# Optimization experiments

Hardware: AMD Instinct MI355X
Metric: run time of the kernel (lower is better)

## Reference

```python
import jax, jax.numpy as jnp
import numpy as np

D_MODEL = 1024
D_INNER = 1024
N_HEADS = 16
HEAD_DIM = D_INNER // N_HEADS  # 64
D_STATE = 16
DT_RANK = 16
CHUNK = 64
PROJ = 2 * D_INNER + 2 * D_STATE * N_HEADS + DT_RANK  # 2576


def setup_inputs() -> dict:
    key = jax.random.key(0)
    ks = jax.random.split(key, 6)
    B, S = 4, 4096
    x = jax.random.normal(ks[0], (B, S, D_MODEL), jnp.float32)
    W_in = jax.random.normal(ks[1], (PROJ, D_MODEL), jnp.float32) * 0.02
    dt_W = jax.random.normal(ks[2], (N_HEADS, DT_RANK), jnp.float32) * 0.1
    dt_b = jax.random.normal(ks[3], (N_HEADS,), jnp.float32) * 0.1
    A_log = jnp.full((N_HEADS,), jnp.log(0.5), jnp.float32)
    D_param = jnp.ones((N_HEADS,), jnp.float32)
    W_out = jax.random.normal(ks[4], (D_MODEL, D_INNER), jnp.float32) * 0.02
    norm_w = jnp.ones((D_INNER,), jnp.float32)
    return dict(x=x, W_in=W_in, dt_W=dt_W, dt_b=dt_b, A_log=A_log,
                D_param=D_param, W_out=W_out, norm_w=norm_w)


def _forward(x, W_in, dt_W, dt_b, A_log, D_param, W_out, norm_w):
    B, S, _ = x.shape
    H, P, N, K = N_HEADS, HEAD_DIM, D_STATE, CHUNK
    proj = x @ W_in.T  # (B,S,PROJ)
    xp = proj[..., :D_INNER]
    z = proj[..., D_INNER:2 * D_INNER]
    o = 2 * D_INNER
    B_ssm = proj[..., o:o + N * H].reshape(B, S, H, N)
    C_ssm = proj[..., o + N * H:o + 2 * N * H].reshape(B, S, H, N)
    dt_low = proj[..., o + 2 * N * H:]
    dt = jax.nn.softplus(dt_low @ dt_W.T + dt_b)  # (B,S,H)
    xp = xp.reshape(B, S, H, P)
    A = -jnp.exp(A_log)  # (H,)

    # --- chunked selective scan (SSD) ---
    nC = S // K  # S chosen divisible by K (original pads otherwise)
    xc = xp.reshape(B, nC, K, H, P)
    dtc = dt.reshape(B, nC, K, H)
    Bc = B_ssm.reshape(B, nC, K, H, N)
    Cc = C_ssm.reshape(B, nC, K, H, N)
    dA = dtc * A  # (B,nC,K,H)
    dAcs = jnp.cumsum(dA, axis=2)
    # intra-chunk quadratic (attention-like) form
    Lm = jnp.exp(dAcs[:, :, :, None, :] - dAcs[:, :, None, :, :])
    causal = jnp.tril(jnp.ones((K, K), jnp.float32))
    Lm = Lm * causal[None, None, :, :, None]
    scores = jnp.einsum('bcihn,bcjhn->bcijh', Cc, Bc) * Lm * dtc[:, :, None, :, :]
    y_intra = jnp.einsum('bcijh,bcjhp->bcihp', scores, xc)
    # per-chunk state contribution
    decay_to_end = jnp.exp(dAcs[:, :, -1:, :] - dAcs)
    wx = (dtc * decay_to_end)[..., None] * xc  # (B,nC,K,H,P)
    chunk_state = jnp.einsum('bckhn,bckhp->bchnp', Bc, wx)  # (B,nC,H,N,P)
    chunk_decay = jnp.exp(dAcs[:, :, -1, :])  # (B,nC,H)

    # cross-chunk recurrence: emit state at chunk START (matches torch loop)
    def step(h, inp):
        d, s = inp
        return d[:, :, None, None] * h + s, h
    h0 = jnp.zeros((B, H, N, P), jnp.float32)
    _, h_states = jax.lax.scan(
        step, h0,
        (jnp.moveaxis(chunk_decay, 1, 0), jnp.moveaxis(chunk_state, 1, 0)))
    h_states = jnp.moveaxis(h_states, 0, 1)  # (B,nC,H,N,P)

    y_cross = jnp.einsum('bcthn,bchnp,bcth->bcthp', Cc, h_states, jnp.exp(dAcs))
    y = (y_intra + y_cross).reshape(B, S, H, P)
    # --- end scan ---

    y = y + xp * D_param[None, None, :, None]
    y = y.reshape(B, S, D_INNER)
    rms = jnp.sqrt(jnp.mean(y * y, axis=-1, keepdims=True) + 1e-6)
    y = y / rms * norm_w
    y = y * jax.nn.silu(z)
    return y @ W_out.T


def reference(x, W_in, dt_W, dt_b, A_log, D_param, W_out, norm_w):
    return _forward(x, W_in, dt_W, dt_b, A_log, D_param, W_out, norm_w)
```

## Files before the change

kernel.cpp:

```cpp
#include <hip/hip_runtime.h>

typedef unsigned short u16;
typedef __attribute__((ext_vector_type(8))) short short8;
typedef __attribute__((ext_vector_type(4))) float f32x4;
typedef __attribute__((ext_vector_type(4))) unsigned short u16x4;
typedef __attribute__((ext_vector_type(8))) unsigned short u16x8;

#define BTOK 16384
#define PROJ_N 2576
#define PROJ_PAD 2816
#define DK 1024
#define NCH 256
#define NH 16
#define HD 64
#define NS 16

__device__ __forceinline__ float b2f(u16 b) {
    union { unsigned int u; float f; } v; v.u = ((unsigned int)b) << 16; return v.f;
}
__device__ __forceinline__ u16 f2b(float f) {
    union { float f; unsigned int u; } v; v.f = f;
    unsigned int r = v.u + 0x7fffu + ((v.u >> 16) & 1u);
    return (u16)(r >> 16);
}

__device__ __forceinline__ void stage_asm(const u16* g, const u16* l) {
    unsigned loff = (unsigned)(size_t)(const __attribute__((address_space(3))) u16*)l;
    unsigned su = __builtin_amdgcn_readfirstlane(loff);
    asm volatile("s_mov_b32 m0, %1\n\t"
                 "global_load_lds_dwordx4 %0, off"
                 :: "v"(g), "s"(su));
}

template <int IMM>
__device__ __forceinline__ short8 dsr128(unsigned a) {
    short8 d;
    asm volatile("ds_read_b128 %0, %1 offset:%2" : "=v"(d) : "v"(a), "i"(IMM));
    return d;
}

#define LGKM(n) do { asm volatile("s_waitcnt lgkmcnt(" #n ")"); __builtin_amdgcn_sched_barrier(0); } while (0)
#define MFMA_B16 __builtin_amdgcn_mfma_f32_16x16x32_bf16

__global__ __launch_bounds__(256) void cast_bf16(const float* __restrict__ s,
                                                 u16* __restrict__ d, int n4) {
    int t = blockIdx.x * 256 + threadIdx.x;
    if (t < n4) {
        float4 v = ((const float4*)s)[t];
        u16x4 o; o.x = f2b(v.x); o.y = f2b(v.y); o.z = f2b(v.z); o.w = f2b(v.w);
        ((u16x4*)d)[t] = o;
    }
}

__global__ __launch_bounds__(256) void cast_pad_win(const float* __restrict__ s,
                                                    u16* __restrict__ d) {
    int t = blockIdx.x * 256 + threadIdx.x;
    int i4 = t * 4;
    float4 v = make_float4(0.f, 0.f, 0.f, 0.f);
    if (i4 < PROJ_N * DK) v = ((const float4*)s)[t];
    u16x4 o; o.x = f2b(v.x); o.y = f2b(v.y); o.z = f2b(v.z); o.w = f2b(v.w);
    ((u16x4*)d)[t] = o;
}

#define MT 64

template <int OUT_BF16>
__global__ __launch_bounds__(512, 2) void gemmk(const u16* __restrict__ A,
                                                const u16* __restrict__ B,
                                                float* __restrict__ Cf,
                                                u16* __restrict__ Cb,
                                                int K, int ldc) {
    extern __shared__ u16 smem[];
    u16* AsU = smem;
    const int tid = threadIdx.x;
    const int wave = tid >> 6, lane = tid & 63;
    const int wr = wave >> 2, wc = wave & 3;
    const int m_l = lane & 15, quad = lane >> 4;

    const int b = blockIdx.x;
    const int bm = (b & 7) * 8 + ((b >> 3) & 7);
    const int bn = b >> 6;

    const u16* Ab = A + (long)bm * 256 * K;
    const u16* Bb = B + (long)bn * 256 * K;

    const unsigned lds0 = (unsigned)(size_t)(const __attribute__((address_space(3))) u16*)smem;
    const int sw = m_l & 7;
    const unsigned a0b = lds0 + (wr * 128 + m_l) * 128 + (quad ^ sw) * 16;
    const unsigned a1b = lds0 + (wr * 128 + m_l) * 128 + ((4 + quad) ^ sw) * 16;
    const unsigned b0b = lds0 + 65536 + (wc * 64 + m_l) * 128 + (quad ^ sw) * 16;
    const unsigned b1b = lds0 + 65536 + (wc * 64 + m_l) * 128 + ((4 + quad) ^ sw) * 16;

    const int srow = tid >> 3;
    const int schk = (tid & 7) ^ (srow & 7);
    const int sdst = wave * 512;

    f32x4 acc[8][4];
#pragma unroll
    for (int f = 0; f < 8; ++f)
#pragma unroll
        for (int n = 0; n < 4; ++n) acc[f][n] = (f32x4){0.f, 0.f, 0.f, 0.f};

    const int NT = K >> 6;

    auto stage = [&](const u16* G, u16* L, int q, int k0) {
        stage_asm(G + (long)(q * 64 + srow) * K + k0 + schk * 8,
                  L + q * 4096 + sdst);
    };
    u16* BsU = smem + 32768;

    stage(Ab, AsU, 0, 0); stage(Ab, AsU, 1, 0); stage(Ab, AsU, 2, 0); stage(Ab, AsU, 3, 0);
    stage(Bb, BsU, 0, 0); stage(Bb, BsU, 1, 0); stage(Bb, BsU, 2, 0); stage(Bb, BsU, 3, 0);
    asm volatile("s_waitcnt vmcnt(0)");
    __builtin_amdgcn_s_barrier();

    short8 afX[4], afY[4], bfX[4], bfY[4];
    afX[0] = dsr128<0>(a0b);    afX[1] = dsr128<2048>(a0b);
    afX[2] = dsr128<4096>(a0b); afX[3] = dsr128<6144>(a0b);
    bfX[0] = dsr128<0>(b0b);    bfX[1] = dsr128<2048>(b0b);
    bfX[2] = dsr128<4096>(b0b); bfX[3] = dsr128<6144>(b0b);

    int cur = 0;
    for (int t = 0; t < NT; ++t) {
        const unsigned cB = ((unsigned)cur) << 15;
        const unsigned a0 = a0b + cB, a1 = a1b + cB, b0 = b0b + cB, b1 = b1b + cB;
        const int nbu = (cur << 14) ^ 16384;
        u16* Anxt = AsU + nbu;
        u16* Bnxt = BsU + nbu;
        const int k1 = (t + 1) << 6;
        const bool s1 = (t + 1 < NT);

        if (s1) { stage(Ab, Anxt, 0, k1); stage(Ab, Anxt, 1, k1); }
        afY[0] = dsr128<8192>(a0);  afY[1] = dsr128<10240>(a0);
        afY[2] = dsr128<12288>(a0); afY[3] = dsr128<14336>(a0);
        LGKM(4);
        __builtin_amdgcn_s_setprio(1);
#pragma unroll
        for (int f = 0; f < 4; ++f)
#pragma unroll
            for (int n = 0; n < 4; ++n)
                acc[f][n] = MFMA_B16(afX[f], bfX[n], acc[f][n], 0, 0, 0);
        __builtin_amdgcn_s_setprio(0);

        if (s1) { stage(Ab, Anxt, 2, k1); stage(Ab, Anxt, 3, k1); }
        afX[0] = dsr128<0>(a1);    afX[1] = dsr128<2048>(a1);
        afX[2] = dsr128<4096>(a1); afX[3] = dsr128<6144>(a1);
        bfY[0] = dsr128<0>(b1);    bfY[1] = dsr128<2048>(b1);
        bfY[2] = dsr128<4096>(b1); bfY[3] = dsr128<6144>(b1);
        LGKM(8);
        __builtin_amdgcn_s_setprio(1);
#pragma unroll
        for (int f = 0; f < 4; ++f)
#pragma unroll
            for (int n = 0; n < 4; ++n)
                acc[4 + f][n] = MFMA_B16(afY[f], bfX[n], acc[4 + f][n], 0, 0, 0);
        __builtin_amdgcn_s_setprio(0);

        if (s1) { stage(Bb, Bnxt, 0, k1); stage(Bb, Bnxt, 1, k1); }
        afY[0] = dsr128<8192>(a1);  afY[1] = dsr128<10240>(a1);
        afY[2] = dsr128<12288>(a1); afY[3] = dsr128<14336>(a1);
        LGKM(4);
        __builtin_amdgcn_s_setprio(1);
#pragma unroll
        for (int f = 0; f < 4; ++f)
#pragma unroll
            for (int n = 0; n < 4; ++n)
                acc[f][n] = MFMA_B16(afX[f], bfY[n], acc[f][n], 0, 0, 0);
        __builtin_amdgcn_s_setprio(0);

        if (s1) { stage(Bb, Bnxt, 2, k1); stage(Bb, Bnxt, 3, k1); }
        LGKM(0);
        __builtin_amdgcn_s_setprio(1);
#pragma unroll
        for (int f = 0; f < 4; ++f)
#pragma unroll
            for (int n = 0; n < 4; ++n)
                acc[4 + f][n] = MFMA_B16(afY[f], bfY[n], acc[4 + f][n], 0, 0, 0);
        __builtin_amdgcn_s_setprio(0);
        __builtin_amdgcn_sched_barrier(0);

        if (s1) {
            asm volatile("s_waitcnt vmcnt(0)");
            __builtin_amdgcn_s_barrier();
            const unsigned nB = cB ^ 32768u;
            const unsigned na0 = a0b + nB, nb0 = b0b + nB;
            afX[0] = dsr128<0>(na0);    afX[1] = dsr128<2048>(na0);
            afX[2] = dsr128<4096>(na0); afX[3] = dsr128<6144>(na0);
            bfX[0] = dsr128<0>(nb0);    bfX[1] = dsr128<2048>(nb0);
            bfX[2] = dsr128<4096>(nb0); bfX[3] = dsr128<6144>(nb0);
        }
        cur ^= 1;
    }

#pragma unroll
    for (int f = 0; f < 8; ++f) {
        int row_base = bm * 256 + wr * 128 + f * 16 + quad * 4;
#pragma unroll
        for (int n = 0; n < 4; ++n) {
            int col = bn * 256 + wc * 64 + n * 16 + m_l;
#pragma unroll
            for (int r = 0; r < 4; ++r) {
                float v = acc[f][n][r];
                long off = (long)(row_base + r) * ldc + col;
                if (OUT_BF16) Cb[off] = f2b(v);
                else          Cf[off] = v;
            }
        }
    }
}

__global__ __launch_bounds__(256) void ssm_intra(const u16* __restrict__ proj,
                                                 const float* __restrict__ dt_W,
                                                 const float* __restrict__ dt_b,
                                                 const float* __restrict__ A_log,
                                                 float* __restrict__ dAcs,
                                                 float* __restrict__ decay,
                                                 u16* __restrict__ y_acc,
                                                 float* __restrict__ cstate) {
    int bch = blockIdx.x;
    int bc = bch >> 4, h = bch & 15;
    long tok0 = (long)bc * 64;
    __shared__ float Cs[64][20], Bm[64][20];
    __shared__ u16 Sh[64][72], Sl[64][72];
    __shared__ u16 Xt[64][72];
    __shared__ u16 Wh[64][72], Wl[64][72];
    __shared__ u16 Bt[16][72];
    __shared__ float dts[64], dAs[64], wk[64];
    const int tid = threadIdx.x;
    const int wave = tid >> 6, lane = tid & 63;
    const int m_l = lane & 15, quad = lane >> 4;

    if (tid < 64) {
        long tok = tok0 + tid;
        u16x8 lo0 = *(const u16x8*)&proj[tok * PROJ_PAD + 2560];
        u16x8 lo1 = *(const u16x8*)&proj[tok * PROJ_PAD + 2568];
        float a = dt_b[h];
#pragma unroll
        for (int r = 0; r < 8; ++r) a += b2f(lo0[r]) * dt_W[h * 16 + r];
#pragma unroll
        for (int r = 0; r < 8; ++r) a += b2f(lo1[r]) * dt_W[h * 16 + 8 + r];
        float d = (a > 20.f) ? a : log1pf(__expf(a));
        float dA = -__expf(A_log[h]) * d;
        float cs = dA;
#pragma unroll
        for (int off = 1; off < 64; off <<= 1) {
            float o = __shfl_up(cs, off, 64);
            if (tid >= off) cs += o;
        }
        float cs63 = __shfl(cs, 63, 64);
        dts[tid] = d;
        dAs[tid] = cs;
        wk[tid] = d * __expf(cs63 - cs);
        dAcs[tok * 16 + h] = cs;
        if (tid == 63) decay[bc * 16 + h] = __expf(cs);
    }
#pragma unroll
    for (int it = 0; it < 4; ++it) {
        int li = it * 256 + tid;
        int i = li >> 4, n = li & 15;
        u16 cb = proj[(tok0 + i) * PROJ_PAD + 2304 + h * 16 + n];
        u16 bb = proj[(tok0 + i) * PROJ_PAD + 2048 + h * 16 + n];
        Cs[i][n] = b2f(cb);
        Bm[i][n] = b2f(bb);
        Bt[n][i] = bb;
    }
    __syncthreads();
#pragma unroll
    for (int it = 0; it < 2; ++it) {
        int li = it * 256 + tid;
        int j = li & 63, p0 = (li >> 6) * 8;
        u16x8 xv = *(const u16x8*)&proj[(tok0 + j) * PROJ_PAD + h * 64 + p0];
        float w = wk[j];
#pragma unroll
        for (int t = 0; t < 8; ++t) {
            u16 xb = xv[t];
            Xt[p0 + t][j] = xb;
            float v = w * b2f(xb);
            u16 hi = f2b(v);
            Wh[p0 + t][j] = hi;
            Wl[p0 + t][j] = f2b(v - b2f(hi));
        }
    }
    {
        int j = tid & 63, i0 = tid >> 6;
#pragma unroll
        for (int g = 0; g < 16; ++g) {
            int i = i0 + g * 4;
            float v = 0.f;
            if (j <= i) {
                float d = 0.f;
                const f32x4* cp = (const f32x4*)Cs[i];
                const f32x4* bp = (const f32x4*)Bm[j];
#pragma unroll
                for (int n4 = 0; n4 < 4; ++n4) {
                    f32x4 c = cp[n4], b = bp[n4];
                    d += c.x * b.x + c.y * b.y + c.z * b.z + c.w * b.w;
                }
                v = d * __expf(dAs[i] - dAs[j]) * dts[j];
            }
            u16 hi = f2b(v);
            Sh[i][j] = hi;
            Sl[i][j] = f2b(v - b2f(hi));
        }
    }
    __syncthreads();
    {
        f32x4 yv[4];
#pragma unroll
        for (int jt = 0; jt < 4; ++jt) yv[jt] = (f32x4){0.f, 0.f, 0.f, 0.f};
#pragma unroll
        for (int ks = 0; ks < 2; ++ks) {
            int kc = ks * 32 + quad * 8;
            short8 ah = *(const short8*)&Sh[wave * 16 + m_l][kc];
            short8 al = *(const short8*)&Sl[wave * 16 + m_l][kc];
#pragma unroll
            for (int jt = 0; jt < 4; ++jt) {
                short8 bx = *(const short8*)&Xt[jt * 16 + m_l][kc];
                yv[jt] = MFMA_B16(ah, bx, yv[jt], 0, 0, 0);
                yv[jt] = MFMA_B16(al, bx, yv[jt], 0, 0, 0);
            }
        }
#pragma unroll
        for (int jt = 0; jt < 4; ++jt)
#pragma unroll
            for (int r = 0; r < 4; ++r) {
                int i = wave * 16 + quad * 4 + r;
                int p = jt * 16 + m_l;
                y_acc[(tok0 + i) * 1024 + h * 64 + p] = f2b(yv[jt][r]);
            }
    }
    {
        f32x4 cacc = (f32x4){0.f, 0.f, 0.f, 0.f};
#pragma unroll
        for (int ks = 0; ks < 2; ++ks) {
            int kc = ks * 32 + quad * 8;
            short8 a = *(const short8*)&Bt[m_l][kc];
            short8 bh = *(const short8*)&Wh[wave * 16 + m_l][kc];
            short8 bl = *(const short8*)&Wl[wave * 16 + m_l][kc];
            cacc = MFMA_B16(a, bh, cacc, 0, 0, 0);
            cacc = MFMA_B16(a, bl, cacc, 0, 0, 0);
        }
#pragma unroll
        for (int r = 0; r < 4; ++r) {
            int n = quad * 4 + r;
            int p = wave * 16 + m_l;
            cstate[(long)bch * 1024 + n * 64 + p] = cacc[r];
        }
    }
}

__global__ __launch_bounds__(256) void scan_chunks(const float* __restrict__ cs,
                                                   const float* __restrict__ decay,
                                                   float* __restrict__ hs) {
    int t = blockIdx.x * 256 + threadIdx.x;
    int p = t & 63, n = (t >> 6) & 15, h = (t >> 10) & 15, b = t >> 14;
    float state = 0.f;
    for (int c = 0; c < 64; ++c) {
        long idx = (((long)((b * 64 + c) * 16 + h)) * 16 + n) * 64 + p;
        hs[idx] = state;
        state = decay[(b * 64 + c) * 16 + h] * state + cs[idx];
    }
}

__global__ __launch_bounds__(256) void ssm_cross(const u16* __restrict__ proj,
                                                 const float* __restrict__ dAcs,
                                                 const float* __restrict__ hs,
                                                 const u16* __restrict__ y_acc,
                                                 const float* __restrict__ D_param,
                                                 u16* __restrict__ y_pre) {
    int bch = blockIdx.x;
    int bc = bch >> 4, h = bch & 15;
    long tok0 = (long)bc * 64;
    __shared__ float hss[16][64], Cs[64][16], dAs[64];
    int tid = threadIdx.x;
#pragma unroll
    for (int it = 0; it < 4; ++it) {
        int li = it * 256 + tid;
        hss[li >> 6][li & 63] = hs[(long)bch * 1024 + li];
        int i = li >> 4, n = li & 15;
        Cs[i][n] = b2f(proj[(tok0 + i) * PROJ_PAD + 2304 + h * 16 + n]);
    }
    if (tid < 64) dAs[tid] = dAcs[(tok0 + tid) * 16 + h];
    __syncthreads();
    float Dh = D_param[h];
    int pi = (tid & 15) * 4;
    int ib = tid >> 4;
#pragma unroll
    for (int g = 0; g < 4; ++g) {
        int i = ib + 16 * g;
        f32x4 cr = (f32x4){0.f, 0.f, 0.f, 0.f};
#pragma unroll
        for (int n = 0; n < 16; ++n) {
            float c = Cs[i][n];
            cr += c * *(const f32x4*)&hss[n][pi];
        }
        float e = __expf(dAs[i]);
        long off = (tok0 + i) * 1024 + h * 64 + pi;
        u16x4 ya = *(const u16x4*)&y_acc[off];
        u16x4 xv = *(const u16x4*)&proj[(tok0 + i) * PROJ_PAD + h * 64 + pi];
        u16x4 o;
        o.x = f2b(b2f(ya.x) + e * cr.x + b2f(xv.x) * Dh);
        o.y = f2b(b2f(ya.y) + e * cr.y + b2f(xv.y) * Dh);
        o.z = f2b(b2f(ya.z) + e * cr.z + b2f(xv.z) * Dh);
        o.w = f2b(b2f(ya.w) + e * cr.w + b2f(xv.w) * Dh);
        *(u16x4*)&y_pre[off] = o;
    }
}

__global__ __launch_bounds__(256) void norm_gate(const u16* __restrict__ proj,
                                                 const float* __restrict__ norm_w,
                                                 u16* __restrict__ y) {
    long tok = blockIdx.x;
    int tid = threadIdx.x;
    int c0 = tid * 4;
    u16x4 yv = *(const u16x4*)&y[tok * 1024 + c0];
    float v0 = b2f(yv.x), v1 = b2f(yv.y), v2 = b2f(yv.z), v3 = b2f(yv.w);
    float ss = v0 * v0 + v1 * v1 + v2 * v2 + v3 * v3;
    int lane = tid & 63, w = tid >> 6;
#pragma unroll
    for (int d = 32; d > 0; d >>= 1) ss += __shfl_down(ss, d, 64);
    __shared__ float red[4];
    if (lane == 0) red[w] = ss;
    __syncthreads();
    float tot = red[0] + red[1] + red[2] + red[3];
    float inv = rsqrtf(tot * (1.f / 1024.f) + 1e-6f);
    float4 nw = *(const float4*)&norm_w[c0];
    u16x4 zv = *(const u16x4*)&proj[tok * PROJ_PAD + 1024 + c0];
    float z0 = b2f(zv.x), z1 = b2f(zv.y), z2 = b2f(zv.z), z3 = b2f(zv.w);
    u16x4 o;
    o.x = f2b(v0 * inv * nw.x * (z0 / (1.f + __expf(-z0))));
    o.y = f2b(v1 * inv * nw.y * (z1 / (1.f + __expf(-z1))));
    o.z = f2b(v2 * inv * nw.z * (z2 / (1.f + __expf(-z2))));
    o.w = f2b(v3 * inv * nw.w * (z3 / (1.f + __expf(-z3))));
    *(u16x4*)&y[tok * 1024 + c0] = o;
}

extern "C" void kernel_launch(void* const* d_in, const int* in_sizes, int n_in,
                              void* d_out, int out_size, void* d_ws, size_t ws_size,
                              hipStream_t stream) {
    const float* x      = (const float*)d_in[0];
    const float* W_in   = (const float*)d_in[1];
    const float* dt_W   = (const float*)d_in[2];
    const float* dt_b   = (const float*)d_in[3];
    const float* A_log  = (const float*)d_in[4];
    const float* D_par  = (const float*)d_in[5];
    const float* W_out  = (const float*)d_in[6];
    const float* norm_w = (const float*)d_in[7];
    float* out = (float*)d_out;

    char* ws = (char*)d_ws;
    size_t off = 0;
    auto alloc = [&](size_t b) { void* p = ws + off; off += (b + 255) & ~(size_t)255; return p; };
    u16*   x_bf    = (u16*)alloc((size_t)BTOK * DK * 2);
    u16*   win_bf  = (u16*)alloc((size_t)PROJ_PAD * DK * 2);
    u16*   wout_bf = (u16*)alloc((size_t)DK * DK * 2);
    u16*   proj    = (u16*)alloc((size_t)BTOK * PROJ_PAD * 2);
    float* dAcs    = (float*)alloc((size_t)BTOK * NH * 4);
    float* decay   = (float*)alloc((size_t)NCH * NH * 4);
    float* cstate  = (float*)alloc((size_t)NCH * NH * NS * HD * 4);
    float* hstates = (float*)alloc((size_t)NCH * NH * NS * HD * 4);
    u16*   y_pre   = (u16*)alloc((size_t)BTOK * DK * 2);
    u16*   y_acc   = x_bf;

    static bool attr_done = false;
    if (!attr_done) {
        (void)hipFuncSetAttribute(reinterpret_cast<const void*>(&gemmk<1>),
                                  hipFuncAttributeMaxDynamicSharedMemorySize, 131072);
        (void)hipFuncSetAttribute(reinterpret_cast<const void*>(&gemmk<0>),
                                  hipFuncAttributeMaxDynamicSharedMemorySize, 131072);
        attr_done = true;
    }

    cast_bf16<<<BTOK * DK / 4 / 256, 256, 0, stream>>>(x, x_bf, BTOK * DK / 4);
    cast_bf16<<<DK * DK / 4 / 256, 256, 0, stream>>>(W_out, wout_bf, DK * DK / 4);
    cast_pad_win<<<PROJ_PAD * DK / 4 / 256, 256, 0, stream>>>(W_in, win_bf);

    gemmk<1><<<dim3(MT * (PROJ_PAD / 256)), 512, 131072, stream>>>(x_bf, win_bf, nullptr, proj, DK, PROJ_PAD);

    ssm_intra<<<NCH * NH, 256, 0, stream>>>(proj, dt_W, dt_b, A_log, dAcs, decay, y_acc, cstate);
    scan_chunks<<<256, 256, 0, stream>>>(cstate, decay, hstates);
    ssm_cross<<<NCH * NH, 256, 0, stream>>>(proj, dAcs, hstates, y_acc, D_par, y_pre);
    norm_gate<<<BTOK, 256, 0, stream>>>(proj, norm_w, y_pre);

    gemmk<0><<<dim3(MT * (DK / 256)), 512, 131072, stream>>>(y_pre, wout_bf, out, nullptr, DK, DK);
}
```

Baseline: 379.0 us.

## Load GEMM A fragments directly from global and shrink tile to 256x128

Replaces the 512-thread 256x256 GEMM, which staged both A and B tiles through 128KB of dynamic LDS, with a 256-thread 256x128 kernel. Each wave now reads its A fragments straight from global memory into registers, and only B goes through a 32KB static LDS double buffer. The projection padding drops from 2816 to 2688 columns so the grid divides by 128, which removes wasted padded compute. The intent is to cut LDS traffic, lower LDS use so more blocks can be resident, and reduce padding work. The cost is uncoalesced, un-shared A loads from global, where each A row segment is fetched by separate waves and blocks, plus less reuse per block.

```diff
diff --git a/kernel.cpp b/kernel.cpp
--- a/kernel.cpp
+++ b/kernel.cpp
@@ -8,7 +8,7 @@
 
 #define BTOK 16384
 #define PROJ_N 2576
-#define PROJ_PAD 2816
+#define PROJ_PAD 2688
 #define DK 1024
 #define NCH 256
 #define NH 16
@@ -41,6 +41,7 @@
 
 #define LGKM(n) do { asm volatile("s_waitcnt lgkmcnt(" #n ")"); __builtin_amdgcn_sched_barrier(0); } while (0)
 #define MFMA_B16 __builtin_amdgcn_mfma_f32_16x16x32_bf16
+#define SB0() __builtin_amdgcn_sched_barrier(0)
 
 __global__ __launch_bounds__(256) void cast_bf16(const float* __restrict__ s,
                                                  u16* __restrict__ d, int n4) {
@@ -65,16 +66,15 @@
 #define MT 64
 
 template <int OUT_BF16>
-__global__ __launch_bounds__(512, 2) void gemmk(const u16* __restrict__ A,
+__global__ __launch_bounds__(256, 2) void gemmf(const u16* __restrict__ A,
                                                 const u16* __restrict__ B,
                                                 float* __restrict__ Cf,
                                                 u16* __restrict__ Cb,
                                                 int K, int ldc) {
-    extern __shared__ u16 smem[];
-    u16* AsU = smem;
+    __shared__ u16 Bs[2 * 128 * 64];
     const int tid = threadIdx.x;
     const int wave = tid >> 6, lane = tid & 63;
-    const int wr = wave >> 2, wc = wave & 3;
+    const int mw = wave >> 1, nw = wave & 1;
     const int m_l = lane & 15, quad = lane >> 4;
 
     const int b = blockIdx.x;
@@ -82,18 +82,18 @@
     const int bn = b >> 6;
 
     const u16* Ab = A + (long)bm * 256 * K;
-    const u16* Bb = B + (long)bn * 256 * K;
-
-    const unsigned lds0 = (unsigned)(size_t)(const __attribute__((address_space(3))) u16*)smem;
+    const u16* Bb = B + (long)bn * 128 * K;
+
+    const u16* ap0 = Ab + (long)(mw * 128 + m_l) * K + quad * 8;
+    const int fstride = 16 * K;
+
+    const unsigned lds0 = (unsigned)(size_t)(const __attribute__((address_space(3))) u16*)Bs;
     const int sw = m_l & 7;
-    const unsigned a0b = lds0 + (wr * 128 + m_l) * 128 + (quad ^ sw) * 16;
-    const unsigned a1b = lds0 + (wr * 128 + m_l) * 128 + ((4 + quad) ^ sw) * 16;
-    const unsigned b0b = lds0 + 65536 + (wc * 64 + m_l) * 128 + (quad ^ sw) * 16;
-    const unsigned b1b = lds0 + 65536 + (wc * 64 + m_l) * 128 + ((4 + quad) ^ sw) * 16;
+    const unsigned b0b = lds0 + (nw * 64 + m_l) * 128 + (quad ^ sw) * 16;
+    const unsigned b1b = lds0 + (nw * 64 + m_l) * 128 + ((4 + quad) ^ sw) * 16;
 
     const int srow = tid >> 3;
     const int schk = (tid & 7) ^ (srow & 7);
-    const int sdst = wave * 512;
 
     f32x4 acc[8][4];
 #pragma unroll
@@ -103,101 +103,73 @@
 
     const int NT = K >> 6;
 
-    auto stage = [&](const u16* G, u16* L, int q, int k0) {
-        stage_asm(G + (long)(q * 64 + srow) * K + k0 + schk * 8,
-                  L + q * 4096 + sdst);
+    auto stageB = [&](unsigned bufU16, int q, int k0) {
+        stage_asm(Bb + (long)(q * 32 + srow) * K + k0 + schk * 8,
+                  Bs + bufU16 + q * 2048 + wave * 512);
     };
-    u16* BsU = smem + 32768;
-
-    stage(Ab, AsU, 0, 0); stage(Ab, AsU, 1, 0); stage(Ab, AsU, 2, 0); stage(Ab, AsU, 3, 0);
-    stage(Bb, BsU, 0, 0); stage(Bb, BsU, 1, 0); stage(Bb, BsU, 2, 0); stage(Bb, BsU, 3, 0);
+
+    stageB(0, 0, 0); stageB(0, 1, 0); stageB(0, 2, 0); stageB(0, 3, 0);
     asm volatile("s_waitcnt vmcnt(0)");
     __builtin_amdgcn_s_barrier();
 
-    short8 afX[4], afY[4], bfX[4], bfY[4];
-    afX[0] = dsr128<0>(a0b);    afX[1] = dsr128<2048>(a0b);
-    afX[2] = dsr128<4096>(a0b); afX[3] = dsr128<6144>(a0b);
+    short8 afX[8], afY[8], bfX[4], bfY[4];
     bfX[0] = dsr128<0>(b0b);    bfX[1] = dsr128<2048>(b0b);
     bfX[2] = dsr128<4096>(b0b); bfX[3] = dsr128<6144>(b0b);
-
-    int cur = 0;
+#pragma unroll
+    for (int f = 0; f < 8; ++f) afX[f] = *(const short8*)(ap0 + f * fstride);
+
+    unsigned curB = 0;
     for (int t = 0; t < NT; ++t) {
-        const unsigned cB = ((unsigned)cur) << 15;
-        const unsigned a0 = a0b + cB, a1 = a1b + cB, b0 = b0b + cB, b1 = b1b + cB;
-        const int nbu = (cur << 14) ^ 16384;
-        u16* Anxt = AsU + nbu;
-        u16* Bnxt = BsU + nbu;
-        const int k1 = (t + 1) << 6;
         const bool s1 = (t + 1 < NT);
-
-        if (s1) { stage(Ab, Anxt, 0, k1); stage(Ab, Anxt, 1, k1); }
-        afY[0] = dsr128<8192>(a0);  afY[1] = dsr128<10240>(a0);
-        afY[2] = dsr128<12288>(a0); afY[3] = dsr128<14336>(a0);
+        const int k0 = t << 6, k1 = (t + 1) << 6;
+
+        bfY[0] = dsr128<0>(b1b + curB);    bfY[1] = dsr128<2048>(b1b + curB);
+        bfY[2] = dsr128<4096>(b1b + curB); bfY[3] = dsr128<6144>(b1b + curB);
+#pragma unroll
+        for (int f = 0; f < 8; ++f) afY[f] = *(const short8*)(ap0 + f * fstride + k0 + 32);
+
+        if (s1) {
+            unsigned nx = (curB >> 1) ^ 8192u;
+            stageB(nx, 0, k1); stageB(nx, 1, k1); stageB(nx, 2, k1); stageB(nx, 3, k1);
+        }
+
         LGKM(4);
         __builtin_amdgcn_s_setprio(1);
 #pragma unroll
-        for (int f = 0; f < 4; ++f)
+        for (int f = 0; f < 8; ++f)
 #pragma unroll
             for (int n = 0; n < 4; ++n)
                 acc[f][n] = MFMA_B16(afX[f], bfX[n], acc[f][n], 0, 0, 0);
         __builtin_amdgcn_s_setprio(0);
-
-        if (s1) { stage(Ab, Anxt, 2, k1); stage(Ab, Anxt, 3, k1); }
-        afX[0] = dsr128<0>(a1);    afX[1] = dsr128<2048>(a1);
-        afX[2] = dsr128<4096>(a1); afX[3] = dsr128<6144>(a1);
-        bfY[0] = dsr128<0>(b1);    bfY[1] = dsr128<2048>(b1);
-        bfY[2] = dsr128<4096>(b1); bfY[3] = dsr128<6144>(b1);
-        LGKM(8);
-        __builtin_amdgcn_s_setprio(1);
-#pragma unroll
-        for (int f = 0; f < 4; ++f)
-#pragma unroll
-            for (int n = 0; n < 4; ++n)
-                acc[4 + f][n] = MFMA_B16(afY[f], bfX[n], acc[4 + f][n], 0, 0, 0);
-        __builtin_amdgcn_s_setprio(0);
-
-        if (s1) { stage(Bb, Bnxt, 0, k1); stage(Bb, Bnxt, 1, k1); }
-        afY[0] = dsr128<8192>(a1);  afY[1] = dsr128<10240>(a1);
-        afY[2] = dsr128<12288>(a1); afY[3] = dsr128<14336>(a1);
-        LGKM(4);
-        __builtin_amdgcn_s_setprio(1);
-#pragma unroll
-        for (int f = 0; f < 4; ++f)
-#pragma unroll
-            for (int n = 0; n < 4; ++n)
-                acc[f][n] = MFMA_B16(afX[f], bfY[n], acc[f][n], 0, 0, 0);
-        __builtin_amdgcn_s_setprio(0);
-
-        if (s1) { stage(Bb, Bnxt, 2, k1); stage(Bb, Bnxt, 3, k1); }
+        SB0();
+
         LGKM(0);
         __builtin_amdgcn_s_setprio(1);
 #pragma unroll
-        for (int f = 0; f < 4; ++f)
+        for (int f = 0; f < 8; ++f)
 #pragma unroll
             for (int n = 0; n < 4; ++n)
-                acc[4 + f][n] = MFMA_B16(afY[f], bfY[n], acc[4 + f][n], 0, 0, 0);
+                acc[f][n] = MFMA_B16(afY[f], bfY[n], acc[f][n], 0, 0, 0);
         __builtin_amdgcn_s_setprio(0);
-        __builtin_amdgcn_sched_barrier(0);
+        SB0();
 
         if (s1) {
             asm volatile("s_waitcnt vmcnt(0)");
             __builtin_amdgcn_s_barrier();
-            const unsigned nB = cB ^ 32768u;
-            const unsigned na0 = a0b + nB, nb0 = b0b + nB;
-            afX[0] = dsr128<0>(na0);    afX[1] = dsr128<2048>(na0);
-            afX[2] = dsr128<4096>(na0); afX[3] = dsr128<6144>(na0);
-            bfX[0] = dsr128<0>(nb0);    bfX[1] = dsr128<2048>(nb0);
-            bfX[2] = dsr128<4096>(nb0); bfX[3] = dsr128<6144>(nb0);
-        }
-        cur ^= 1;
+            curB ^= 16384u;
+            bfX[0] = dsr128<0>(b0b + curB);    bfX[1] = dsr128<2048>(b0b + curB);
+            bfX[2] = dsr128<4096>(b0b + curB); bfX[3] = dsr128<6144>(b0b + curB);
+#pragma unroll
+            for (int f = 0; f < 8; ++f) afX[f] = *(const short8*)(ap0 + f * fstride + k1);
+        }
     }
 
 #pragma unroll
     for (int f = 0; f < 8; ++f) {
-        int row_base = bm * 256 + wr * 128 + f * 16 + quad * 4;
+        int row_base = bm * 256 + mw * 128 + f * 16 + quad * 4;
 #pragma unroll
         for (int n = 0; n < 4; ++n) {
-            int col = bn * 256 + wc * 64 + n * 16 + m_l;
+            int col = bn * 128 + nw * 64 + n * 16 + m_l;
 #pragma unroll
             for (int r = 0; r < 4; ++r) {
                 float v = acc[f][n][r];
@@ -462,25 +434,16 @@
     u16*   y_pre   = (u16*)alloc((size_t)BTOK * DK * 2);
     u16*   y_acc   = x_bf;
 
-    static bool attr_done = false;
-    if (!attr_done) {
-        (void)hipFuncSetAttribute(reinterpret_cast<const void*>(&gemmk<1>),
-                                  hipFuncAttributeMaxDynamicSharedMemorySize, 131072);
-        (void)hipFuncSetAttribute(reinterpret_cast<const void*>(&gemmk<0>),
-                                  hipFuncAttributeMaxDynamicSharedMemorySize, 131072);
-        attr_done = true;
-    }
-
     cast_bf16<<<BTOK * DK / 4 / 256, 256, 0, stream>>>(x, x_bf, BTOK * DK / 4);
     cast_bf16<<<DK * DK / 4 / 256, 256, 0, stream>>>(W_out, wout_bf, DK * DK / 4);
     cast_pad_win<<<PROJ_PAD * DK / 4 / 256, 256, 0, stream>>>(W_in, win_bf);
 
-    gemmk<1><<<dim3(MT * (PROJ_PAD / 256)), 512, 131072, stream>>>(x_bf, win_bf, nullptr, proj, DK, PROJ_PAD);
+    gemmf<1><<<dim3(MT * (PROJ_PAD / 128)), 256, 0, stream>>>(x_bf, win_bf, nullptr, proj, DK, PROJ_PAD);
 
     ssm_intra<<<NCH * NH, 256, 0, stream>>>(proj, dt_W, dt_b, A_log, dAcs, decay, y_acc, cstate);
     scan_chunks<<<256, 256, 0, stream>>>(cstate, decay, hstates);
     ssm_cross<<<NCH * NH, 256, 0, stream>>>(proj, dAcs, hstates, y_acc, D_par, y_pre);
     norm_gate<<<BTOK, 256, 0, stream>>>(proj, norm_w, y_pre);
 
-    gemmk<0><<<dim3(MT * (DK / 256)), 512, 131072, stream>>>(y_pre, wout_bf, out, nullptr, DK, DK);
-}
+    gemmf<0><<<dim3(MT * (DK / 128)), 256, 0, stream>>>(y_pre, wout_bf, out, nullptr, DK, DK);
+}
```

Result: slower. 546.1 us (+44.1%).

## Fuse cross-chunk state output with RMSNorm and SiLU gate into one kernel

Applied to the files above, without the earlier changes.

Replaces the separate ssm_cross and norm_gate kernels with a single cross_norm kernel. Each 1024-thread block handles one 64-token chunk across all 16 heads, holds the pre-norm outputs in registers, reduces the per-token sum of squares through LDS, then applies the norm and gate. This removes one kernel launch and the write and re-read of the pre-norm y buffer. In exchange the grid shrinks to 256 large blocks with heavy LDS use (about 107 KB), which limits occupancy and latency hiding.

```diff
diff --git a/kernel.cpp b/kernel.cpp
--- a/kernel.cpp
+++ b/kernel.cpp
@@ -362,39 +362,57 @@
     }
 }
 
-__global__ __launch_bounds__(256) void ssm_cross(const u16* __restrict__ proj,
-                                                 const float* __restrict__ dAcs,
-                                                 const float* __restrict__ hs,
-                                                 const u16* __restrict__ y_acc,
-                                                 const float* __restrict__ D_param,
-                                                 u16* __restrict__ y_pre) {
-    int bch = blockIdx.x;
-    int bc = bch >> 4, h = bch & 15;
-    long tok0 = (long)bc * 64;
-    __shared__ float hss[16][64], Cs[64][16], dAs[64];
-    int tid = threadIdx.x;
-#pragma unroll
-    for (int it = 0; it < 4; ++it) {
-        int li = it * 256 + tid;
-        hss[li >> 6][li & 63] = hs[(long)bch * 1024 + li];
-        int i = li >> 4, n = li & 15;
-        Cs[i][n] = b2f(proj[(tok0 + i) * PROJ_PAD + 2304 + h * 16 + n]);
-    }
-    if (tid < 64) dAs[tid] = dAcs[(tok0 + tid) * 16 + h];
+#define CN_LDS (65536 + 32768 + 4352 + 4352 + 256)
+
+__global__ __launch_bounds__(1024, 1) void cross_norm(const u16* __restrict__ proj,
+                                                      const float* __restrict__ dAcs,
+                                                      const float* __restrict__ hs,
+                                                      const u16* __restrict__ y_acc,
+                                                      const float* __restrict__ D_param,
+                                                      const float* __restrict__ norm_w,
+                                                      u16* __restrict__ y) {
+    extern __shared__ char cnl[];
+    float* hss  = (float*)cnl;
+    u16*   Csl  = (u16*)(cnl + 65536);
+    float* dAe  = (float*)(cnl + 65536 + 32768);
+    float* ssl  = dAe + 64 * 17;
+    float* invv = ssl + 64 * 17;
+    const int bc = blockIdx.x;
+    const long tok0 = (long)bc * 64;
+    const int tid = threadIdx.x;
+    const int h = tid >> 6, l = tid & 63;
+
+    {
+        long base = (long)bc * 16384;
+#pragma unroll
+        for (int it = 0; it < 16; ++it)
+            hss[it * 1024 + tid] = hs[base + it * 1024 + tid];
+    }
+    {
+        int i = tid >> 4, hh = tid & 15;
+        const u16* cp = &proj[(tok0 + i) * PROJ_PAD + 2304 + hh * 16];
+        u16x8 c0 = *(const u16x8*)cp;
+        u16x8 c1 = *(const u16x8*)(cp + 8);
+        *(u16x8*)&Csl[(i * 16 + hh) * 16] = c0;
+        *(u16x8*)&Csl[(i * 16 + hh) * 16 + 8] = c1;
+        dAe[i * 17 + hh] = __expf(dAcs[(tok0 + i) * 16 + hh]);
+    }
     __syncthreads();
-    float Dh = D_param[h];
-    int pi = (tid & 15) * 4;
-    int ib = tid >> 4;
-#pragma unroll
-    for (int g = 0; g < 4; ++g) {
-        int i = ib + 16 * g;
+
+    const float Dh = D_param[h];
+    const int pi = (l & 15) * 4;
+    const int ib = l >> 4;
+    u16x4 yv[16];
+
+#pragma unroll
+    for (int g = 0; g < 16; ++g) {
+        int i = ib + 4 * g;
         f32x4 cr = (f32x4){0.f, 0.f, 0.f, 0.f};
-#pragma unroll
-        for (int n = 0; n < 16; ++n) {
-            float c = Cs[i][n];
-            cr += c * *(const f32x4*)&hss[n][pi];
-        }
-        float e = __expf(dAs[i]);
+        const u16* Cp = &Csl[(i * 16 + h) * 16];
+#pragma unroll
+        for (int n = 0; n < 16; ++n)
+            cr += b2f(Cp[n]) * *(const f32x4*)&hss[(h * 16 + n) * 64 + pi];
+        float e = dAe[i * 17 + h];
         long off = (tok0 + i) * 1024 + h * 64 + pi;
         u16x4 ya = *(const u16x4*)&y_acc[off];
         u16x4 xv = *(const u16x4*)&proj[(tok0 + i) * PROJ_PAD + h * 64 + pi];
@@ -403,36 +421,37 @@
         o.y = f2b(b2f(ya.y) + e * cr.y + b2f(xv.y) * Dh);
         o.z = f2b(b2f(ya.z) + e * cr.z + b2f(xv.z) * Dh);
         o.w = f2b(b2f(ya.w) + e * cr.w + b2f(xv.w) * Dh);
-        *(u16x4*)&y_pre[off] = o;
-    }
-}
-
-__global__ __launch_bounds__(256) void norm_gate(const u16* __restrict__ proj,
-                                                 const float* __restrict__ norm_w,
-                                                 u16* __restrict__ y) {
-    long tok = blockIdx.x;
-    int tid = threadIdx.x;
-    int c0 = tid * 4;
-    u16x4 yv = *(const u16x4*)&y[tok * 1024 + c0];
-    float v0 = b2f(yv.x), v1 = b2f(yv.y), v2 = b2f(yv.z), v3 = b2f(yv.w);
-    float ss = v0 * v0 + v1 * v1 + v2 * v2 + v3 * v3;
-    int lane = tid & 63, w = tid >> 6;
-#pragma unroll
-    for (int d = 32; d > 0; d >>= 1) ss += __shfl_down(ss, d, 64);
-    __shared__ float red[4];
-    if (lane == 0) red[w] = ss;
+        yv[g] = o;
+        float v0 = b2f(o.x), v1 = b2f(o.y), v2 = b2f(o.z), v3 = b2f(o.w);
+        float ss = v0 * v0 + v1 * v1 + v2 * v2 + v3 * v3;
+#pragma unroll
+        for (int d = 1; d < 16; d <<= 1) ss += __shfl_xor(ss, d, 16);
+        if ((l & 15) == 0) ssl[i * 17 + h] = ss;
+    }
     __syncthreads();
-    float tot = red[0] + red[1] + red[2] + red[3];
-    float inv = rsqrtf(tot * (1.f / 1024.f) + 1e-6f);
-    float4 nw = *(const float4*)&norm_w[c0];
-    u16x4 zv = *(const u16x4*)&proj[tok * PROJ_PAD + 1024 + c0];
-    float z0 = b2f(zv.x), z1 = b2f(zv.y), z2 = b2f(zv.z), z3 = b2f(zv.w);
-    u16x4 o;
-    o.x = f2b(v0 * inv * nw.x * (z0 / (1.f + __expf(-z0))));
-    o.y = f2b(v1 * inv * nw.y * (z1 / (1.f + __expf(-z1))));
-    o.z = f2b(v2 * inv * nw.z * (z2 / (1.f + __expf(-z2))));
-    o.w = f2b(v3 * inv * nw.w * (z3 / (1.f + __expf(-z3))));
-    *(u16x4*)&y[tok * 1024 + c0] = o;
+    if (tid < 64) {
+        float s = 0.f;
+#pragma unroll
+        for (int hh = 0; hh < 16; ++hh) s += ssl[tid * 17 + hh];
+        invv[tid] = rsqrtf(s * (1.f / 1024.f) + 1e-6f);
+    }
+    __syncthreads();
+
+    const float4 nw = *(const float4*)&norm_w[h * 64 + pi];
+#pragma unroll
+    for (int g = 0; g < 16; ++g) {
+        int i = ib + 4 * g;
+        float inv = invv[i];
+        long off = (tok0 + i) * 1024 + h * 64 + pi;
+        u16x4 zv = *(const u16x4*)&proj[(tok0 + i) * PROJ_PAD + 1024 + h * 64 + pi];
+        float z0 = b2f(zv.x), z1 = b2f(zv.y), z2 = b2f(zv.z), z3 = b2f(zv.w);
+        u16x4 o;
+        o.x = f2b(b2f(yv[g].x) * inv * nw.x * (z0 / (1.f + __expf(-z0))));
+        o.y = f2b(b2f(yv[g].y) * inv * nw.y * (z1 / (1.f + __expf(-z1))));
+        o.z = f2b(b2f(yv[g].z) * inv * nw.z * (z2 / (1.f + __expf(-z2))));
+        o.w = f2b(b2f(yv[g].w) * inv * nw.w * (z3 / (1.f + __expf(-z3))));
+        *(u16x4*)&y[off] = o;
+    }
 }
 
 extern "C" void kernel_launch(void* const* d_in, const int* in_sizes, int n_in,
@@ -468,6 +487,8 @@
                                   hipFuncAttributeMaxDynamicSharedMemorySize, 131072);
         (void)hipFuncSetAttribute(reinterpret_cast<const void*>(&gemmk<0>),
                                   hipFuncAttributeMaxDynamicSharedMemorySize, 131072);
+        (void)hipFuncSetAttribute(reinterpret_cast<const void*>(&cross_norm),
+                                  hipFuncAttributeMaxDynamicSharedMemorySize, CN_LDS);
         attr_done = true;
     }
 
@@ -479,8 +500,7 @@
 
     ssm_intra<<<NCH * NH, 256, 0, stream>>>(proj, dt_W, dt_b, A_log, dAcs, decay, y_acc, cstate);
     scan_chunks<<<256, 256, 0, stream>>>(cstate, decay, hstates);
-    ssm_cross<<<NCH * NH, 256, 0, stream>>>(proj, dAcs, hstates, y_acc, D_par, y_pre);
-    norm_gate<<<BTOK, 256, 0, stream>>>(proj, norm_w, y_pre);
+    cross_norm<<<NCH, 1024, CN_LDS, stream>>>(proj, dAcs, hstates, y_acc, D_par, norm_w, y_pre);
 
     gemmk<0><<<dim3(MT * (DK / 256)), 512, 131072, stream>>>(y_pre, wout_bf, out, nullptr, DK, DK);
 }
```

Measured after the change: 390.9 us. 3.1% more time.
